# Optimization experiments

Hardware: AMD Instinct MI355X
Metric: run time of the kernel (lower is better)

## Reference

```python
import jax, jax.numpy as jnp
import numpy as np

B, L, D, E, H, TOP_K = 4, 2048, 1024, 8, 512, 2

def setup_inputs() -> dict:
    key = jax.random.key(0)
    k = jax.random.split(key, 6)
    x = jax.random.normal(k[0], (B, L, D), dtype=jnp.float32)
    gate_w = jax.random.normal(k[1], (D, E), dtype=jnp.float32) * 0.02
    gate_b = jnp.zeros((E,), jnp.float32)
    w1 = jax.random.normal(k[2], (E, D, H), dtype=jnp.float32) * 0.02
    b1 = jnp.zeros((E, H), jnp.float32)
    w2 = jax.random.normal(k[3], (E, H, D), dtype=jnp.float32) * 0.02
    b2 = jnp.zeros((E, D), jnp.float32)
    return {"x": x, "gate_w": gate_w, "gate_b": gate_b,
            "w1": w1, "b1": b1, "w2": w2, "b2": b2}

def reference(x, gate_w, gate_b, w1, b1, w2, b2):
    b, l, d = x.shape
    e = gate_w.shape[1]
    xf = x.reshape(-1, d)                      # [T, D], T = B*L
    t = xf.shape[0]
    # gating (eval mode: clean logits, no noise)
    logits = xf @ gate_w + gate_b              # [T, E]
    top_vals, top_idx = jax.lax.top_k(logits, TOP_K)
    top_gates = jax.nn.softmax(top_vals, axis=-1)
    gates = jnp.zeros((t, e), x.dtype).at[jnp.arange(t)[:, None], top_idx].set(top_gates)
    # per-expert 2-layer MLP computed densely, combined with sparse gates
    h = jax.nn.gelu(jnp.einsum('td,edh->eth', xf, w1) + b1[:, None, :], approximate=False)
    eo = jnp.einsum('eth,ehd->etd', h, w2) + b2[:, None, :]   # [E, T, D]
    out = jnp.einsum('te,etd->td', gates, eo)                 # weighted combine
    return out.reshape(b, l, d)
```

## Files before the change

### kernel.cpp

```cpp
#include <hip/hip_runtime.h>
#include <hip/hip_bf16.h>
#include <stdint.h>

#define B_    4
#define L_    2048
#define T_    8192
#define D_    1024
#define E_    8
#define H_    512

typedef __bf16  bf16x8 __attribute__((ext_vector_type(8)));
typedef float   f32x4  __attribute__((ext_vector_type(4)));
typedef unsigned short ushort_t;

__device__ __forceinline__ ushort_t f2bf(float f) {
    union { float f; unsigned u; } v; v.f = f;
    unsigned u = v.u;
    unsigned r = (u + 0x7fffu + ((u >> 16) & 1u)) >> 16;
    return (ushort_t)r;
}

__device__ __forceinline__ float gelu_exact(float v) {
    return 0.5f * v * (1.0f + erff(v * 0.70710678118654752f));
}

__device__ __forceinline__ void gld_lds16(const void* g, void* l) {
    __attribute__((address_space(3))) uint32_t* lp =
        reinterpret_cast<__attribute__((address_space(3))) uint32_t*>(
            reinterpret_cast<uintptr_t>(l));
    const __attribute__((address_space(1))) uint32_t* gp =
        reinterpret_cast<const __attribute__((address_space(1))) uint32_t*>(
            reinterpret_cast<uintptr_t>(g));
    __builtin_amdgcn_global_load_lds(gp, lp, 16, 0, 0);
}

__global__ __launch_bounds__(256) void transpose_cvt2(
    const float* __restrict__ w1, const float* __restrict__ w2,
    ushort_t* __restrict__ o1, ushort_t* __restrict__ o2)
{
    __shared__ float tile[32][33];
    const int mz = blockIdx.y;
    const float* src; ushort_t* dst; int C, R, sh;
    if (mz < E_) {
        src = w1 + (size_t)mz * D_ * H_; dst = o1 + (size_t)mz * D_ * H_;
        R = D_; C = H_; sh = 4;
    } else {
        const int m = mz - E_;
        src = w2 + (size_t)m * D_ * H_;  dst = o2 + (size_t)m * D_ * H_;
        R = H_; C = D_; sh = 5;
    }
    const int bx = blockIdx.x & ((1 << sh) - 1);
    const int by = blockIdx.x >> sh;
    const int r0 = by * 32, c0 = bx * 32;
    const int tid = threadIdx.x;
    const int lr = tid >> 3;
    const int lc = (tid & 7) * 4;
    float4 v = *(const float4*)(src + (size_t)(r0 + lr) * C + c0 + lc);
    tile[lr][lc+0] = v.x; tile[lr][lc+1] = v.y;
    tile[lr][lc+2] = v.z; tile[lr][lc+3] = v.w;
    __syncthreads();
    ushort4 o;
    o.x = f2bf(tile[lc+0][lr]);
    o.y = f2bf(tile[lc+1][lr]);
    o.z = f2bf(tile[lc+2][lr]);
    o.w = f2bf(tile[lc+3][lr]);
    *(ushort4*)(dst + (size_t)(c0 + lr) * R + r0 + lc) = o;
}

__global__ __launch_bounds__(256) void gating_kernel(
    const float* __restrict__ x, const float* __restrict__ gw,
    const float* __restrict__ gb,
    int* __restrict__ eidx, float* __restrict__ gsel, ushort_t* __restrict__ xbf)
{
    const int wave = threadIdx.x >> 6;
    const int lane = threadIdx.x & 63;
    const int t = blockIdx.x * 4 + wave;
    const float* xr = x + (size_t)t * D_;
    ushort_t* xbr = xbf + (size_t)t * D_;

    float acc[E_];
    #pragma unroll
    for (int e = 0; e < E_; ++e) acc[e] = 0.f;

    #pragma unroll
    for (int j = 0; j < 4; ++j) {
        const int d = j * 256 + lane * 4;
        float4 xv = *(const float4*)(xr + d);
        ushort4 o;
        o.x = f2bf(xv.x); o.y = f2bf(xv.y); o.z = f2bf(xv.z); o.w = f2bf(xv.w);
        *(ushort4*)(xbr + d) = o;
        const float* gr = gw + (size_t)d * E_;
        float xs[4] = {xv.x, xv.y, xv.z, xv.w};
        #pragma unroll
        for (int c = 0; c < 4; ++c) {
            float4 g0 = *(const float4*)(gr + c * 8);
            float4 g1 = *(const float4*)(gr + c * 8 + 4);
            acc[0] += xs[c] * g0.x; acc[1] += xs[c] * g0.y;
            acc[2] += xs[c] * g0.z; acc[3] += xs[c] * g0.w;
            acc[4] += xs[c] * g1.x; acc[5] += xs[c] * g1.y;
            acc[6] += xs[c] * g1.z; acc[7] += xs[c] * g1.w;
        }
    }
    #pragma unroll
    for (int s = 1; s < 64; s <<= 1) {
        #pragma unroll
        for (int e = 0; e < E_; ++e)
            acc[e] += __shfl_xor(acc[e], s, 64);
    }
    if (lane == 0) {
        float v[E_];
        #pragma unroll
        for (int e = 0; e < E_; ++e) v[e] = acc[e] + gb[e];
        int i0 = 0;
        #pragma unroll
        for (int e = 1; e < E_; ++e) if (v[e] > v[i0]) i0 = e;
        int i1 = (i0 == 0) ? 1 : 0;
        #pragma unroll
        for (int e = 0; e < E_; ++e) if (e != i0 && v[e] > v[i1]) i1 = e;
        float g0 = 1.f / (1.f + expf(v[i1] - v[i0]));
        eidx[t] = i0 | (i1 << 8);
        gsel[t] = g0;
    }
}

__global__ __launch_bounds__(256) void bucket_kernel(
    const int* __restrict__ eidx, const float* __restrict__ gsel,
    int* __restrict__ counts, int* __restrict__ btok, float* __restrict__ bgate,
    uint32_t* __restrict__ tpos)
{
    __shared__ int lcnt[E_];
    __shared__ int lbase[E_];
    const int tid = threadIdx.x;
    if (tid < E_) lcnt[tid] = 0;
    __syncthreads();
    const int t = blockIdx.x * 256 + tid;
    const int pk = eidx[t];
    const float g0 = gsel[t];
    const int i0 = pk & 0xff, i1 = (pk >> 8) & 0xff;
    const int p0 = atomicAdd(&lcnt[i0], 1);
    const int p1 = atomicAdd(&lcnt[i1], 1);
    __syncthreads();
    if (tid < E_) lbase[tid] = atomicAdd(&counts[tid], lcnt[tid]);
    __syncthreads();
    const int q0 = lbase[i0] + p0, q1 = lbase[i1] + p1;
    btok[i0 * T_ + q0] = t; bgate[i0 * T_ + q0] = g0;
    btok[i1 * T_ + q1] = t; bgate[i1 * T_ + q1] = 1.f - g0;
    tpos[t] = (uint32_t)((i0 << 13) | q0) | ((uint32_t)((i1 << 13) | q1) << 16);
}

__global__ void prefix_kernel(const int* __restrict__ counts, int* __restrict__ offsets)
{
    if (threadIdx.x == 0 && blockIdx.x == 0) {
        int s = 0;
        for (int e = 0; e < E_; ++e) { offsets[e] = s; s += counts[e]; }
    }
}

__global__ __launch_bounds__(256) void mlp1_kernel(
    const ushort_t* __restrict__ xbf, const ushort_t* __restrict__ w1t,
    const float* __restrict__ b1,
    const int* __restrict__ counts, const int* __restrict__ offsets,
    const int* __restrict__ btok, ushort_t* __restrict__ hbuf)
{
    const int e   = blockIdx.z;
    const int n_e = counts[e];
    const int m0  = blockIdx.x * 64;
    if (m0 >= n_e) return;
    const int n0  = blockIdx.y * 128;
    const int off = offsets[e];

    __shared__ ushort_t As[2][64 * 64];
    __shared__ ushort_t Bs[2][128 * 64];

    const int tid  = threadIdx.x;
    const int lane = tid & 63;
    const int wave = tid >> 6;

    const int srow = tid >> 3;
    const int cg   = (tid & 7) ^ (srow & 7);

    const ushort_t* aptr[2];
    #pragma unroll
    for (int i = 0; i < 2; ++i) {
        int m = m0 + i * 32 + srow;
        int tok = btok[e * T_ + (m < n_e ? m : n_e - 1)];
        aptr[i] = xbf + (size_t)tok * D_ + cg * 8;
    }
    const ushort_t* w1e = w1t + (size_t)e * (H_ * D_);
    const ushort_t* bptr[4];
    #pragma unroll
    for (int i = 0; i < 4; ++i)
        bptr[i] = w1e + (size_t)(n0 + i * 32 + srow) * D_ + cg * 8;

    const int fm   = lane & 15;
    const int quad = lane >> 4;
    const int wm   = (wave & 1) * 32;
    const int wn   = (wave >> 1) * 64;

    f32x4 acc[2][4];
    #pragma unroll
    for (int i = 0; i < 2; ++i)
        #pragma unroll
        for (int j = 0; j < 4; ++j)
            { acc[i][j][0]=0.f; acc[i][j][1]=0.f; acc[i][j][2]=0.f; acc[i][j][3]=0.f; }

    #define STAGE1(bufi, koff)                                              \
        do {                                                                \
            char* al_ = (char*)(&As[bufi][0]) + (wave << 10);               \
            char* bl_ = (char*)(&Bs[bufi][0]) + (wave << 10);               \
            _Pragma("unroll")                                               \
            for (int i_ = 0; i_ < 2; ++i_)                                  \
                gld_lds16(aptr[i_] + (koff), al_ + (i_ << 12));             \
            _Pragma("unroll")                                               \
            for (int i_ = 0; i_ < 4; ++i_)                                  \
                gld_lds16(bptr[i_] + (koff), bl_ + (i_ << 12));             \
        } while (0)

    STAGE1(0, 0);
    __syncthreads();

    int buf = 0;
    for (int k0 = 0; k0 < D_; k0 += 64) {
        const bool more = (k0 + 64 < D_);
        if (more) STAGE1(buf ^ 1, k0 + 64);
        const char* Ab = (const char*)(&As[buf][0]);
        const char* Bb = (const char*)(&Bs[buf][0]);
        #pragma unroll
        for (int kk = 0; kk < 2; ++kk) {
            const int grp = kk * 4 + quad;
            bf16x8 af[2], bfr[4];
            #pragma unroll
            for (int i = 0; i < 2; ++i) {
                int ra = wm + i * 16 + fm;
                af[i]  = *(const bf16x8*)(Ab + ra * 128 + ((grp ^ (ra & 7)) << 4));
            }
            #pragma unroll
            for (int j = 0; j < 4; ++j) {
                int rb = wn + j * 16 + fm;
                bfr[j] = *(const bf16x8*)(Bb + rb * 128 + ((grp ^ (rb & 7)) << 4));
            }
            #pragma unroll
            for (int i = 0; i < 2; ++i)
                #pragma unroll
                for (int j = 0; j < 4; ++j)
                    acc[i][j] = __builtin_amdgcn_mfma_f32_16x16x32_bf16(af[i], bfr[j], acc[i][j], 0, 0, 0);
        }
        if (more) __syncthreads();
        buf ^= 1;
    }
    #undef STAGE1

    float bcol[4];
    #pragma unroll
    for (int j = 0; j < 4; ++j)
        bcol[j] = b1[e * H_ + n0 + wn + j * 16 + fm];
    #pragma unroll
    for (int i = 0; i < 2; ++i) {
        #pragma unroll
        for (int r = 0; r < 4; ++r) {
            int m = m0 + wm + i * 16 + quad * 4 + r;
            if (m >= n_e) continue;
            ushort_t* hrow = hbuf + (size_t)(off + m) * H_ + n0;
            #pragma unroll
            for (int j = 0; j < 4; ++j)
                hrow[wn + j * 16 + fm] = f2bf(gelu_exact(acc[i][j][r] + bcol[j]));
        }
    }
}

__global__ __launch_bounds__(256) void mlp2_kernel(
    const ushort_t* __restrict__ hbuf, const ushort_t* __restrict__ w2t,
    const float* __restrict__ b2,
    const int* __restrict__ counts, const int* __restrict__ offsets,
    const float* __restrict__ bgate, ushort_t* __restrict__ obuf)
{
    const int e   = blockIdx.z;
    const int n_e = counts[e];
    const int m0  = blockIdx.x * 64;
    if (m0 >= n_e) return;
    const int n0  = blockIdx.y * 128;
    const int off = offsets[e];

    __shared__ ushort_t As[2][64 * 64];
    __shared__ ushort_t Bs[2][128 * 64];

    const int tid  = threadIdx.x;
    const int lane = tid & 63;
    const int wave = tid >> 6;

    const int srow = tid >> 3;
    const int cg   = (tid & 7) ^ (srow & 7);

    const ushort_t* aptr[2];
    #pragma unroll
    for (int i = 0; i < 2; ++i)
        aptr[i] = hbuf + (size_t)(off + m0 + i * 32 + srow) * H_ + cg * 8;
    const ushort_t* w2e = w2t + (size_t)e * (D_ * H_);
    const ushort_t* bptr[4];
    #pragma unroll
    for (int i = 0; i < 4; ++i)
        bptr[i] = w2e + (size_t)(n0 + i * 32 + srow) * H_ + cg * 8;

    const int fm   = lane & 15;
    const int quad = lane >> 4;
    const int wm   = (wave & 1) * 32;
    const int wn   = (wave >> 1) * 64;

    f32x4 acc[2][4];
    #pragma unroll
    for (int i = 0; i < 2; ++i)
        #pragma unroll
        for (int j = 0; j < 4; ++j)
            { acc[i][j][0]=0.f; acc[i][j][1]=0.f; acc[i][j][2]=0.f; acc[i][j][3]=0.f; }

    #define STAGE2(bufi, koff)                                              \
        do {                                                                \
            char* al_ = (char*)(&As[bufi][0]) + (wave << 10);               \
            char* bl_ = (char*)(&Bs[bufi][0]) + (wave << 10);               \
            _Pragma("unroll")                                               \
            for (int i_ = 0; i_ < 2; ++i_)                                  \
                gld_lds16(aptr[i_] + (koff), al_ + (i_ << 12));             \
            _Pragma("unroll")                                               \
            for (int i_ = 0; i_ < 4; ++i_)                                  \
                gld_lds16(bptr[i_] + (koff), bl_ + (i_ << 12));             \
        } while (0)

    STAGE2(0, 0);
    __syncthreads();

    int buf = 0;
    for (int k0 = 0; k0 < H_; k0 += 64) {
        const bool more = (k0 + 64 < H_);
        if (more) STAGE2(buf ^ 1, k0 + 64);
        const char* Ab = (const char*)(&As[buf][0]);
        const char* Bb = (const char*)(&Bs[buf][0]);
        #pragma unroll
        for (int kk = 0; kk < 2; ++kk) {
            const int grp = kk * 4 + quad;
            bf16x8 af[2], bfr[4];
            #pragma unroll
            for (int i = 0; i < 2; ++i) {
                int ra = wm + i * 16 + fm;
                af[i]  = *(const bf16x8*)(Ab + ra * 128 + ((grp ^ (ra & 7)) << 4));
            }
            #pragma unroll
            for (int j = 0; j < 4; ++j) {
                int rb = wn + j * 16 + fm;
                bfr[j] = *(const bf16x8*)(Bb + rb * 128 + ((grp ^ (rb & 7)) << 4));
            }
            #pragma unroll
            for (int i = 0; i < 2; ++i)
                #pragma unroll
                for (int j = 0; j < 4; ++j)
                    acc[i][j] = __builtin_amdgcn_mfma_f32_16x16x32_bf16(af[i], bfr[j], acc[i][j], 0, 0, 0);
        }
        if (more) __syncthreads();
        buf ^= 1;
    }
    #undef STAGE2

    float bcol[4];
    #pragma unroll
    for (int j = 0; j < 4; ++j)
        bcol[j] = b2[e * D_ + n0 + wn + j * 16 + fm];
    #pragma unroll
    for (int i = 0; i < 2; ++i) {
        #pragma unroll
        for (int r = 0; r < 4; ++r) {
            int m = m0 + wm + i * 16 + quad * 4 + r;
            if (m >= n_e) continue;
            float g = bgate[e * T_ + m];
            ushort_t* orow = obuf + (size_t)(off + m) * D_ + n0;
            #pragma unroll
            for (int j = 0; j < 4; ++j)
                orow[wn + j * 16 + fm] = f2bf((acc[i][j][r] + bcol[j]) * g);
        }
    }
}

__global__ __launch_bounds__(256) void combine_kernel(
    const ushort_t* __restrict__ obuf, const uint32_t* __restrict__ tpos,
    const int* __restrict__ offsets, float* __restrict__ out)
{
    const int tid = threadIdx.x;
    const int t = blockIdx.x * 2 + (tid >> 7);
    const int c = (tid & 127) * 8;
    const uint32_t pk = tpos[t];
    const int e0 = (pk >> 13) & 7, p0 = pk & 0x1fff;
    const int e1 = (pk >> 29) & 7, p1 = (pk >> 16) & 0x1fff;
    const size_t s0 = (size_t)(offsets[e0] + p0) * D_ + c;
    const size_t s1 = (size_t)(offsets[e1] + p1) * D_ + c;
    bf16x8 a = *(const bf16x8*)(obuf + s0);
    bf16x8 b = *(const bf16x8*)(obuf + s1);
    float4 o0, o1;
    o0.x = (float)a[0] + (float)b[0];
    o0.y = (float)a[1] + (float)b[1];
    o0.z = (float)a[2] + (float)b[2];
    o0.w = (float)a[3] + (float)b[3];
    o1.x = (float)a[4] + (float)b[4];
    o1.y = (float)a[5] + (float)b[5];
    o1.z = (float)a[6] + (float)b[6];
    o1.w = (float)a[7] + (float)b[7];
    float* orow = out + (size_t)t * D_ + c;
    *(float4*)(orow)     = o0;
    *(float4*)(orow + 4) = o1;
}

extern "C" void kernel_launch(void* const* d_in, const int* in_sizes, int n_in,
                              void* d_out, int out_size, void* d_ws, size_t ws_size,
                              hipStream_t stream)
{
    const float* x  = (const float*)d_in[0];
    const float* gw = (const float*)d_in[1];
    const float* gb = (const float*)d_in[2];
    const float* w1 = (const float*)d_in[3];
    const float* b1 = (const float*)d_in[4];
    const float* w2 = (const float*)d_in[5];
    const float* b2 = (const float*)d_in[6];
    float* out = (float*)d_out;

    char* ws = (char*)d_ws;
    int*   counts  = (int*)ws;
    int*   offsets = counts + 8;
    int*   btok    = (int*)(ws + 256);
    float* bgate   = (float*)(ws + 256 + (size_t)E_*T_*4);
    size_t p = 256 + 2ull * E_ * T_ * 4;
    int*      eidx = (int*)(ws + p);      p += (size_t)T_ * 4;
    float*    gsel = (float*)(ws + p);    p += (size_t)T_ * 4;
    uint32_t* tpos = (uint32_t*)(ws + p); p += (size_t)T_ * 4;
    ushort_t* xbf  = (ushort_t*)(ws + p); p += (size_t)T_*D_*2;
    ushort_t* w1t  = (ushort_t*)(ws + p); p += (size_t)E_*H_*D_*2;
    ushort_t* w2t  = (ushort_t*)(ws + p); p += (size_t)E_*D_*H_*2;
    ushort_t* hbuf = (ushort_t*)(ws + p); p += ((size_t)2*T_+128)*H_*2;
    ushort_t* obuf = (ushort_t*)(ws + p);

    (void)hipMemsetAsync(counts, 0, 64, stream);

    transpose_cvt2<<<dim3(512, 16), 256, 0, stream>>>(w1, w2, w1t, w2t);
    gating_kernel<<<T_/4, 256, 0, stream>>>(x, gw, gb, eidx, gsel, xbf);
    bucket_kernel<<<T_/256, 256, 0, stream>>>(eidx, gsel, counts, btok, bgate, tpos);
    prefix_kernel<<<1, 64, 0, stream>>>(counts, offsets);
    mlp1_kernel<<<dim3(T_/64, H_/128, E_), 256, 0, stream>>>(
        xbf, w1t, b1, counts, offsets, btok, hbuf);
    mlp2_kernel<<<dim3(T_/64, D_/128, E_), 256, 0, stream>>>(
        hbuf, w2t, b2, counts, offsets, bgate, obuf);
    combine_kernel<<<T_/2, 256, 0, stream>>>(obuf, tpos, offsets, out);
}
```

Baseline: 232.2 us.

## Deepen GEMM prefetch pipeline, stage gate weights in LDS, drop prefix kernel

```diff
diff --git a/kernel.cpp b/kernel.cpp
--- a/kernel.cpp
+++ b/kernel.cpp
@@ -72,54 +72,68 @@
     const float* __restrict__ gb,
     int* __restrict__ eidx, float* __restrict__ gsel, ushort_t* __restrict__ xbf)
 {
-    const int wave = threadIdx.x >> 6;
-    const int lane = threadIdx.x & 63;
-    const int t = blockIdx.x * 4 + wave;
-    const float* xr = x + (size_t)t * D_;
-    ushort_t* xbr = xbf + (size_t)t * D_;
-
-    float acc[E_];
-    #pragma unroll
-    for (int e = 0; e < E_; ++e) acc[e] = 0.f;
-
-    #pragma unroll
-    for (int j = 0; j < 4; ++j) {
-        const int d = j * 256 + lane * 4;
-        float4 xv = *(const float4*)(xr + d);
-        ushort4 o;
-        o.x = f2bf(xv.x); o.y = f2bf(xv.y); o.z = f2bf(xv.z); o.w = f2bf(xv.w);
-        *(ushort4*)(xbr + d) = o;
-        const float* gr = gw + (size_t)d * E_;
-        float xs[4] = {xv.x, xv.y, xv.z, xv.w};
-        #pragma unroll
-        for (int c = 0; c < 4; ++c) {
-            float4 g0 = *(const float4*)(gr + c * 8);
-            float4 g1 = *(const float4*)(gr + c * 8 + 4);
-            acc[0] += xs[c] * g0.x; acc[1] += xs[c] * g0.y;
-            acc[2] += xs[c] * g0.z; acc[3] += xs[c] * g0.w;
-            acc[4] += xs[c] * g1.x; acc[5] += xs[c] * g1.y;
-            acc[6] += xs[c] * g1.z; acc[7] += xs[c] * g1.w;
-        }
-    }
-    #pragma unroll
-    for (int s = 1; s < 64; s <<= 1) {
-        #pragma unroll
-        for (int e = 0; e < E_; ++e)
-            acc[e] += __shfl_xor(acc[e], s, 64);
-    }
-    if (lane == 0) {
-        float v[E_];
-        #pragma unroll
-        for (int e = 0; e < E_; ++e) v[e] = acc[e] + gb[e];
-        int i0 = 0;
-        #pragma unroll
-        for (int e = 1; e < E_; ++e) if (v[e] > v[i0]) i0 = e;
-        int i1 = (i0 == 0) ? 1 : 0;
-        #pragma unroll
-        for (int e = 0; e < E_; ++e) if (e != i0 && v[e] > v[i1]) i1 = e;
-        float g0 = 1.f / (1.f + expf(v[i1] - v[i0]));
-        eidx[t] = i0 | (i1 << 8);
-        gsel[t] = g0;
+    __shared__ float gwT[E_][D_];
+    const int tid = threadIdx.x;
+
+    #pragma unroll
+    for (int it = 0; it < 8; ++it) {
+        const int idx = it * 256 + tid;
+        float4 v = *(const float4*)(gw + (size_t)idx * 4);
+        const int row = idx >> 1;
+        const int col = (idx & 1) * 4;
+        gwT[col+0][row] = v.x;
+        gwT[col+1][row] = v.y;
+        gwT[col+2][row] = v.z;
+        gwT[col+3][row] = v.w;
+    }
+    __syncthreads();
+
+    const int wave = tid >> 6;
+    const int lane = tid & 63;
+
+    #pragma unroll
+    for (int it = 0; it < 2; ++it) {
+        const int t = blockIdx.x * 8 + wave * 2 + it;
+        const float* xr = x + (size_t)t * D_;
+        ushort_t* xbr = xbf + (size_t)t * D_;
+
+        float acc[E_];
+        #pragma unroll
+        for (int e = 0; e < E_; ++e) acc[e] = 0.f;
+
+        #pragma unroll
+        for (int j = 0; j < 4; ++j) {
+            const int d = j * 256 + lane * 4;
+            float4 xv = *(const float4*)(xr + d);
+            ushort4 o;
+            o.x = f2bf(xv.x); o.y = f2bf(xv.y); o.z = f2bf(xv.z); o.w = f2bf(xv.w);
+            *(ushort4*)(xbr + d) = o;
+            #pragma unroll
+            for (int e = 0; e < E_; ++e) {
+                float4 w = *(const float4*)(&gwT[e][d]);
+                acc[e] += xv.x * w.x + xv.y * w.y + xv.z * w.z + xv.w * w.w;
+            }
+        }
+        #pragma unroll
+        for (int s = 1; s < 64; s <<= 1) {
+            #pragma unroll
+            for (int e = 0; e < E_; ++e)
+                acc[e] += __shfl_xor(acc[e], s, 64);
+        }
+        if (lane == 0) {
+            float v[E_];
+            #pragma unroll
+            for (int e = 0; e < E_; ++e) v[e] = acc[e] + gb[e];
+            int i0 = 0;
+            #pragma unroll
+            for (int e = 1; e < E_; ++e) if (v[e] > v[i0]) i0 = e;
+            int i1 = (i0 == 0) ? 1 : 0;
+            #pragma unroll
+            for (int e = 0; e < E_; ++e) if (e != i0 && v[e] > v[i1]) i1 = e;
+            float g0 = 1.f / (1.f + expf(v[i1] - v[i0]));
+            eidx[t] = i0 | (i1 << 8);
+            gsel[t] = g0;
+        }
     }
 }
 
@@ -148,26 +162,19 @@
     tpos[t] = (uint32_t)((i0 << 13) | q0) | ((uint32_t)((i1 << 13) | q1) << 16);
 }
 
-__global__ void prefix_kernel(const int* __restrict__ counts, int* __restrict__ offsets)
-{
-    if (threadIdx.x == 0 && blockIdx.x == 0) {
-        int s = 0;
-        for (int e = 0; e < E_; ++e) { offsets[e] = s; s += counts[e]; }
-    }
-}
-
 __global__ __launch_bounds__(256) void mlp1_kernel(
     const ushort_t* __restrict__ xbf, const ushort_t* __restrict__ w1t,
     const float* __restrict__ b1,
-    const int* __restrict__ counts, const int* __restrict__ offsets,
+    const int* __restrict__ counts,
     const int* __restrict__ btok, ushort_t* __restrict__ hbuf)
 {
     const int e   = blockIdx.z;
     const int n_e = counts[e];
     const int m0  = blockIdx.x * 64;
     if (m0 >= n_e) return;
+    int off = 0;
+    for (int i = 0; i < e; ++i) off += counts[i];
     const int n0  = blockIdx.y * 128;
-    const int off = offsets[e];
 
     __shared__ ushort_t As[2][64 * 64];
     __shared__ ushort_t Bs[2][128 * 64];
@@ -217,12 +224,15 @@
         } while (0)
 
     STAGE1(0, 0);
-    __syncthreads();
+    __builtin_amdgcn_sched_barrier(0);
+    STAGE1(1, 64);
+    __builtin_amdgcn_sched_barrier(0);
 
     int buf = 0;
     for (int k0 = 0; k0 < D_; k0 += 64) {
-        const bool more = (k0 + 64 < D_);
-        if (more) STAGE1(buf ^ 1, k0 + 64);
+        if (k0 + 64 < D_) asm volatile("s_waitcnt vmcnt(6)" ::: "memory");
+        else              asm volatile("s_waitcnt vmcnt(0)" ::: "memory");
+        __builtin_amdgcn_s_barrier();
         const char* Ab = (const char*)(&As[buf][0]);
         const char* Bb = (const char*)(&Bs[buf][0]);
         #pragma unroll
@@ -245,7 +255,12 @@
                 for (int j = 0; j < 4; ++j)
                     acc[i][j] = __builtin_amdgcn_mfma_f32_16x16x32_bf16(af[i], bfr[j], acc[i][j], 0, 0, 0);
         }
-        if (more) __syncthreads();
+        if (k0 + 128 < D_) {
+            asm volatile("s_waitcnt lgkmcnt(0)" ::: "memory");
+            __builtin_amdgcn_s_barrier();
+            STAGE1(buf, k0 + 128);
+            __builtin_amdgcn_sched_barrier(0);
+        }
         buf ^= 1;
     }
     #undef STAGE1
@@ -271,15 +286,16 @@
 __global__ __launch_bounds__(256) void mlp2_kernel(
     const ushort_t* __restrict__ hbuf, const ushort_t* __restrict__ w2t,
     const float* __restrict__ b2,
-    const int* __restrict__ counts, const int* __restrict__ offsets,
+    const int* __restrict__ counts,
     const float* __restrict__ bgate, ushort_t* __restrict__ obuf)
 {
     const int e   = blockIdx.z;
     const int n_e = counts[e];
     const int m0  = blockIdx.x * 64;
     if (m0 >= n_e) return;
+    int off = 0;
+    for (int i = 0; i < e; ++i) off += counts[i];
     const int n0  = blockIdx.y * 128;
-    const int off = offsets[e];
 
     __shared__ ushort_t As[2][64 * 64];
     __shared__ ushort_t Bs[2][128 * 64];
@@ -326,12 +342,15 @@
         } while (0)
 
     STAGE2(0, 0);
-    __syncthreads();
+    __builtin_amdgcn_sched_barrier(0);
+    STAGE2(1, 64);
+    __builtin_amdgcn_sched_barrier(0);
 
     int buf = 0;
     for (int k0 = 0; k0 < H_; k0 += 64) {
-        const bool more = (k0 + 64 < H_);
-        if (more) STAGE2(buf ^ 1, k0 + 64);
+        if (k0 + 64 < H_) asm volatile("s_waitcnt vmcnt(6)" ::: "memory");
+        else              asm volatile("s_waitcnt vmcnt(0)" ::: "memory");
+        __builtin_amdgcn_s_barrier();
         const char* Ab = (const char*)(&As[buf][0]);
         const char* Bb = (const char*)(&Bs[buf][0]);
         #pragma unroll
@@ -354,7 +373,12 @@
                 for (int j = 0; j < 4; ++j)
                     acc[i][j] = __builtin_amdgcn_mfma_f32_16x16x32_bf16(af[i], bfr[j], acc[i][j], 0, 0, 0);
         }
-        if (more) __syncthreads();
+        if (k0 + 128 < H_) {
+            asm volatile("s_waitcnt lgkmcnt(0)" ::: "memory");
+            __builtin_amdgcn_s_barrier();
+            STAGE2(buf, k0 + 128);
+            __builtin_amdgcn_sched_barrier(0);
+        }
         buf ^= 1;
     }
     #undef STAGE2
@@ -380,7 +404,7 @@
 
 __global__ __launch_bounds__(256) void combine_kernel(
     const ushort_t* __restrict__ obuf, const uint32_t* __restrict__ tpos,
-    const int* __restrict__ offsets, float* __restrict__ out)
+    const int* __restrict__ counts, float* __restrict__ out)
 {
     const int tid = threadIdx.x;
     const int t = blockIdx.x * 2 + (tid >> 7);
@@ -388,8 +412,27 @@
     const uint32_t pk = tpos[t];
     const int e0 = (pk >> 13) & 7, p0 = pk & 0x1fff;
     const int e1 = (pk >> 29) & 7, p1 = (pk >> 16) & 0x1fff;
-    const size_t s0 = (size_t)(offsets[e0] + p0) * D_ + c;
-    const size_t s1 = (size_t)(offsets[e1] + p1) * D_ + c;
+
+    const int4 ca = *(const int4*)(counts);
+    const int4 cb = *(const int4*)(counts + 4);
+    int pre[8];
+    pre[0] = 0;
+    pre[1] = ca.x;
+    pre[2] = pre[1] + ca.y;
+    pre[3] = pre[2] + ca.z;
+    pre[4] = pre[3] + ca.w;
+    pre[5] = pre[4] + cb.x;
+    pre[6] = pre[5] + cb.y;
+    pre[7] = pre[6] + cb.z;
+    int off0 = 0, off1 = 0;
+    #pragma unroll
+    for (int i = 1; i < 8; ++i) {
+        off0 = (e0 == i) ? pre[i] : off0;
+        off1 = (e1 == i) ? pre[i] : off1;
+    }
+
+    const size_t s0 = (size_t)(off0 + p0) * D_ + c;
+    const size_t s1 = (size_t)(off1 + p1) * D_ + c;
     bf16x8 a = *(const bf16x8*)(obuf + s0);
     bf16x8 b = *(const bf16x8*)(obuf + s1);
     float4 o0, o1;
@@ -421,7 +464,6 @@
 
     char* ws = (char*)d_ws;
     int*   counts  = (int*)ws;
-    int*   offsets = counts + 8;
     int*   btok    = (int*)(ws + 256);
     float* bgate   = (float*)(ws + 256 + (size_t)E_*T_*4);
     size_t p = 256 + 2ull * E_ * T_ * 4;
@@ -437,12 +479,11 @@
     (void)hipMemsetAsync(counts, 0, 64, stream);
 
     transpose_cvt2<<<dim3(512, 16), 256, 0, stream>>>(w1, w2, w1t, w2t);
-    gating_kernel<<<T_/4, 256, 0, stream>>>(x, gw, gb, eidx, gsel, xbf);
+    gating_kernel<<<T_/8, 256, 0, stream>>>(x, gw, gb, eidx, gsel, xbf);
     bucket_kernel<<<T_/256, 256, 0, stream>>>(eidx, gsel, counts, btok, bgate, tpos);
-    prefix_kernel<<<1, 64, 0, stream>>>(counts, offsets);
     mlp1_kernel<<<dim3(T_/64, H_/128, E_), 256, 0, stream>>>(
-        xbf, w1t, b1, counts, offsets, btok, hbuf);
+        xbf, w1t, b1, counts, btok, hbuf);
     mlp2_kernel<<<dim3(T_/64, D_/128, E_), 256, 0, stream>>>(
-        hbuf, w2t, b2, counts, offsets, bgate, obuf);
-    combine_kernel<<<T_/2, 256, 0, stream>>>(obuf, tpos, offsets, out);
-}
+        hbuf, w2t, b2, counts, bgate, obuf);
+    combine_kernel<<<T_/2, 256, 0, stream>>>(obuf, tpos, counts, out);
+}
```

New measurement: 214.0 us. -7.8%, faster.
